# Performance work log

Hardware: AMD Instinct MI355X
Metric: run time of the kernel (lower is better)

The kernel has to match this reference:

```python
import jax, jax.numpy as jnp
import numpy as np

H = 1024          # hidden_size
I = 2048          # intermediate_size
E = 8             # num_experts
K = 2             # num_experts_per_token
B, S = 4, 4096


def setup_inputs() -> dict:
    key = jax.random.key(0)
    ks = jax.random.split(key, 5)
    scale = 0.02
    return {
        "hidden_states": jax.random.normal(ks[0], (B, S, H), dtype=jnp.float32),
        "gate_w": jax.random.normal(ks[1], (H, E), dtype=jnp.float32) * scale,      # router gate (Linear, no bias), stored [in,out]
        "gate_proj_w": jax.random.normal(ks[2], (E, H, I), dtype=jnp.float32) * scale,
        "up_proj_w": jax.random.normal(ks[3], (E, H, I), dtype=jnp.float32) * scale,
        "down_proj_w": jax.random.normal(ks[4], (E, I, H), dtype=jnp.float32) * scale,
    }


def reference(hidden_states, gate_w, gate_proj_w, up_proj_w, down_proj_w):
    b, s, h = hidden_states.shape
    x = hidden_states.reshape(-1, h)                      # (T, H), T = b*s
    T = x.shape[0]

    # --- Router: softmax over experts, top-k, renormalize ---
    logits = x @ gate_w                                    # (T, E)
    probs = jax.nn.softmax(logits, axis=-1)
    topk_w, topk_idx = jax.lax.top_k(probs, K)             # (T, K)
    topk_w = topk_w / jnp.sum(topk_w, axis=-1, keepdims=True)

    # Per-token combine weight for each expert (0 if not routed).
    # topk indices are distinct, so scatter-add == scatter-set here.
    combine = jnp.zeros((T, E), dtype=x.dtype).at[
        jnp.arange(T)[:, None], topk_idx
    ].add(topk_w)                                          # (T, E)

    # --- Experts: SwiGLU FFN, weighted combine ---
    out = jnp.zeros_like(x)
    for e in range(E):  # small fixed expert count
        g = jax.nn.silu(x @ gate_proj_w[e])                # (T, I)
        u = x @ up_proj_w[e]                               # (T, I)
        y = (g * u) @ down_proj_w[e]                       # (T, H)
        out = out + y * combine[:, e:e + 1]
    return out.reshape(b, s, h)
```

## Files before the change

kernel.cpp:

```cpp
#include <hip/hip_runtime.h>
#include <hip/hip_bf16.h>

#define T_TOK 16384
#define H_DIM 1024
#define I_DIM 2048
#define E_NUM 8

typedef short short8 __attribute__((ext_vector_type(8)));
typedef float f32x4 __attribute__((ext_vector_type(4)));

__device__ __forceinline__ unsigned short f2bf(float f) {
  union { float f; unsigned u; } v; v.f = f;
  unsigned r = (v.u + 0x7FFFu + ((v.u >> 16) & 1u)) >> 16;
  return (unsigned short)r;
}
__device__ __forceinline__ float bf2f(unsigned short u) {
  union { unsigned u; float f; } v; v.u = ((unsigned)u) << 16;
  return v.f;
}

__device__ __forceinline__ void gload16(const void* g, void* l) {
  __builtin_amdgcn_global_load_lds(
      (const __attribute__((address_space(1))) unsigned int*)g,
      (__attribute__((address_space(3))) unsigned int*)l, 16, 0, 0);
}

#define VMCNT4() asm volatile("s_waitcnt vmcnt(4)" ::: "memory")
#define VMCNT0() asm volatile("s_waitcnt vmcnt(0)" ::: "memory")
#define BAR() __builtin_amdgcn_s_barrier()
#define SCHEDFENCE() __builtin_amdgcn_sched_barrier(0)
#define PRIO1() __builtin_amdgcn_s_setprio(1)
#define PRIO0() __builtin_amdgcn_s_setprio(0)

__global__ __launch_bounds__(256) void convert_router_kernel(
    const float* __restrict__ x, const float* __restrict__ gw,
    unsigned short* __restrict__ xb,
    int* __restrict__ tke, float* __restrict__ pwv) {
  const int tid = threadIdx.x;
  const int lane = tid & 63;
  const int wv = tid >> 6;
  const int t = blockIdx.x * 4 + wv;
  const float* xr = x + (size_t)t * H_DIM;
  unsigned short* xbr = xb + (size_t)t * H_DIM;

  float acc[8] = {0.f, 0.f, 0.f, 0.f, 0.f, 0.f, 0.f, 0.f};
#pragma unroll
  for (int i = 0; i < 16; ++i) {
    const int h = i * 64 + lane;
    float xv = xr[h];
    xbr[h] = f2bf(xv);
    const float4 g0 = *(const float4*)(gw + (size_t)h * 8);
    const float4 g1 = *(const float4*)(gw + (size_t)h * 8 + 4);
    acc[0] += xv * g0.x; acc[1] += xv * g0.y;
    acc[2] += xv * g0.z; acc[3] += xv * g0.w;
    acc[4] += xv * g1.x; acc[5] += xv * g1.y;
    acc[6] += xv * g1.z; acc[7] += xv * g1.w;
  }
#pragma unroll
  for (int e = 0; e < 8; ++e) {
#pragma unroll
    for (int off = 32; off; off >>= 1) acc[e] += __shfl_xor(acc[e], off);
  }
  int e1 = 0; float l1 = acc[0];
#pragma unroll
  for (int e = 1; e < 8; ++e) if (acc[e] > l1) { l1 = acc[e]; e1 = e; }
  int first_non = (e1 == 0) ? 1 : 0;
  int e2 = first_non; float l2 = acc[first_non];
#pragma unroll
  for (int e = 0; e < 8; ++e) {
    if (e == e1 || e == first_non) continue;
    if (acc[e] > l2) { l2 = acc[e]; e2 = e; }
  }
  float r = expf(l2 - l1);
  float w1 = 1.f / (1.f + r);
  float w2 = r / (1.f + r);
  if (lane == 0) {
    pwv[2 * t] = w1;
    pwv[2 * t + 1] = w2;
    tke[t] = e1 | (e2 << 4);
  }
}

__global__ __launch_bounds__(256) void build_lists_kernel(
    const int* __restrict__ tke, int* __restrict__ list, int* __restrict__ cnt) {
  const int t = blockIdx.x * 256 + threadIdx.x;
  const int lane = threadIdx.x & 63;
  const int pk = tke[t];
  const int ee[2] = {pk & 15, (pk >> 4) & 15};
#pragma unroll
  for (int phase = 0; phase < 2; ++phase) {
    const int e = ee[phase];
    const int pid = 2 * t + phase;
#pragma unroll
    for (int ex = 0; ex < E_NUM; ++ex) {
      unsigned long long mask = __ballot(e == ex);
      if (e == ex) {
        unsigned long long below = mask & ((1ull << lane) - 1ull);
        int rank = __popcll(below);
        int leader = __ffsll((unsigned long long)mask) - 1;
        int base = 0;
        if (lane == leader) base = atomicAdd(&cnt[ex], __popcll(mask));
        base = __shfl(base, leader);
        list[ex * T_TOK + base + rank] = pid;
      }
    }
  }
}

__global__ __launch_bounds__(256) void transpose_convert(
    const float* __restrict__ src, unsigned short* __restrict__ dst, int K, int N) {
  __shared__ float t[128][65];
  const int e = blockIdx.x, kt = blockIdx.y, nt = blockIdx.z;
  const float* s = src + (size_t)e * K * N + (size_t)(kt * 128) * N + nt * 64;
  unsigned short* d = dst + (size_t)e * N * K + (size_t)(nt * 64) * K + kt * 128;
  const int tid = threadIdx.x;
  const int lr = tid & 15, row = tid >> 4;
#pragma unroll
  for (int p = 0; p < 8; ++p) {
    int k = row + p * 16;
    float4 v = *(const float4*)(s + (size_t)k * N + lr * 4);
    t[k][lr * 4 + 0] = v.x;
    t[k][lr * 4 + 1] = v.y;
    t[k][lr * 4 + 2] = v.z;
    t[k][lr * 4 + 3] = v.w;
  }
  __syncthreads();
  const int kc = tid & 15, nr = tid >> 4;
#pragma unroll
  for (int p = 0; p < 4; ++p) {
    int n = nr + p * 16;
    short8 o;
#pragma unroll
    for (int j = 0; j < 8; ++j) o[j] = (short)f2bf(t[kc * 8 + j][n]);
    *(short8*)&d[(size_t)n * K + kc * 8] = o;
  }
}

__global__ __launch_bounds__(256, 3) void gemm_gateup(
    const unsigned short* __restrict__ xb, const unsigned short* __restrict__ wgt,
    const unsigned short* __restrict__ wut, const int* __restrict__ list,
    const int* __restrict__ cnt, const float* __restrict__ pwv,
    unsigned short* __restrict__ hbuf) {
  __shared__ unsigned short As[2][128 * 32];
  __shared__ unsigned short Bg[2][64 * 32];
  __shared__ unsigned short Bu[2][64 * 32];
  __shared__ int rows_s[128];
  __shared__ float pws[128];

  const int tid = threadIdx.x;
  const int e = blockIdx.y >> 7;
  const int mt = blockIdx.y & 127;
  const int ce = cnt[e];
  if (mt * 128 >= ce) return;
  const int n0 = blockIdx.x * 64;

  if (tid < 128) {
    int idx = mt * 128 + tid;
    int pid = list[e * T_TOK + (idx < ce ? idx : 0)];
    rows_s[tid] = pid;
    pws[tid] = pwv[pid];
  }
  __syncthreads();

  const int s0 = tid, s1 = 256 + tid;
  const int q0 = (((s0 & 3) ^ ((s0 >> 3) & 3)) * 8);
  const int q1 = (((s1 & 3) ^ ((s1 >> 3) & 3)) * 8);
  const int tok0 = rows_s[s0 >> 2] >> 1, tok1 = rows_s[s1 >> 2] >> 1;

  const unsigned short* wg_base = wgt + ((size_t)e * I_DIM + n0) * H_DIM;
  const unsigned short* wu_base = wut + ((size_t)e * I_DIM + n0) * H_DIM;
  const unsigned short* a_src0 = xb + (size_t)tok0 * H_DIM + q0;
  const unsigned short* a_src1 = xb + (size_t)tok1 * H_DIM + q1;
  const unsigned short* g_src0 = wg_base + (size_t)(s0 >> 2) * H_DIM + q0;
  const unsigned short* u_src0 = wu_base + (size_t)(s0 >> 2) * H_DIM + q0;

#define STAGE_GU(b, k0)                         \
  do {                                          \
    gload16(a_src0 + (k0), &As[b][s0 * 8]);     \
    gload16(a_src1 + (k0), &As[b][s1 * 8]);     \
    gload16(g_src0 + (k0), &Bg[b][s0 * 8]);     \
    gload16(u_src0 + (k0), &Bu[b][s0 * 8]);     \
  } while (0)

  f32x4 zero = {0.f, 0.f, 0.f, 0.f};
  f32x4 accg[4][2], accu[4][2];
#pragma unroll
  for (int m = 0; m < 4; ++m)
#pragma unroll
    for (int n = 0; n < 2; ++n) { accg[m][n] = zero; accu[m][n] = zero; }

  const int lane = tid & 63;
  const int wv = tid >> 6;
  const int wr = (wv >> 1) * 64;
  const int wc = (wv & 1) * 32;
  const int lr = lane & 15;
  const int lks = (((lane >> 4) ^ ((lr >> 1) & 3)) * 8);

  STAGE_GU(0, 0);

  for (int kt = 0; kt < H_DIM / 32; ++kt) {
    const int cur = kt & 1;
    if (kt < H_DIM / 32 - 1) {
      STAGE_GU(cur ^ 1, (kt + 1) * 32);
      VMCNT4();
    } else {
      VMCNT0();
    }
    BAR();
    SCHEDFENCE();
    const unsigned short* Ab = As[cur];
    const unsigned short* Bgb = Bg[cur];
    const unsigned short* Bub = Bu[cur];
    short8 a[4], bg[2], bu[2];
#pragma unroll
    for (int m = 0; m < 4; ++m)
      a[m] = *(const short8*)&Ab[(wr + m * 16 + lr) * 32 + lks];
#pragma unroll
    for (int n = 0; n < 2; ++n) {
      bg[n] = *(const short8*)&Bgb[(wc + n * 16 + lr) * 32 + lks];
      bu[n] = *(const short8*)&Bub[(wc + n * 16 + lr) * 32 + lks];
    }
    PRIO1();
#pragma unroll
    for (int m = 0; m < 4; ++m)
#pragma unroll
      for (int n = 0; n < 2; ++n) {
        accg[m][n] = __builtin_amdgcn_mfma_f32_16x16x32_bf16(a[m], bg[n], accg[m][n], 0, 0, 0);
        accu[m][n] = __builtin_amdgcn_mfma_f32_16x16x32_bf16(a[m], bu[n], accu[m][n], 0, 0, 0);
      }
    PRIO0();
    BAR();
  }
#undef STAGE_GU

  const int rr = (lane >> 4) * 4;
#pragma unroll
  for (int m = 0; m < 4; ++m) {
#pragma unroll
    for (int j = 0; j < 4; ++j) {
      int tr = wr + m * 16 + rr + j;
      if (mt * 128 + tr < ce) {
        int pid = rows_s[tr];
        float wgt_r = pws[tr];
        size_t rowb = (size_t)pid * I_DIM + n0 + wc;
#pragma unroll
        for (int n = 0; n < 2; ++n) {
          float g = accg[m][n][j];
          float u = accu[m][n][j];
          float hv = wgt_r * (g / (1.f + __expf(-g))) * u;
          hbuf[rowb + n * 16 + lr] = f2bf(hv);
        }
      }
    }
  }
}

__global__ __launch_bounds__(256, 3) void gemm_down(
    const unsigned short* __restrict__ hbuf, const unsigned short* __restrict__ wdt,
    const int* __restrict__ list, const int* __restrict__ cnt,
    unsigned short* __restrict__ pbuf) {
  __shared__ unsigned short As[3][128 * 32];
  __shared__ unsigned short Bs[3][128 * 32];
  __shared__ int rows_s[128];

  const int tid = threadIdx.x;
  const int e = blockIdx.y >> 7;
  const int mt = blockIdx.y & 127;
  const int ce = cnt[e];
  if (mt * 128 >= ce) return;
  const int n0 = blockIdx.x * 128;

  if (tid < 128) {
    int idx = mt * 128 + tid;
    rows_s[tid] = list[e * T_TOK + (idx < ce ? idx : 0)];
  }
  __syncthreads();

  const int s0 = tid, s1 = 256 + tid;
  const int r0s = s0 >> 2, r1s = s1 >> 2;
  const int q0 = (((s0 & 3) ^ ((s0 >> 3) & 3)) * 8);
  const int q1 = (((s1 & 3) ^ ((s1 >> 3) & 3)) * 8);
  const int pid0 = rows_s[r0s], pid1 = rows_s[r1s];

  const unsigned short* wd_base = wdt + ((size_t)e * H_DIM + n0) * I_DIM;
  const unsigned short* a_src0 = hbuf + (size_t)pid0 * I_DIM + q0;
  const unsigned short* a_src1 = hbuf + (size_t)pid1 * I_DIM + q1;
  const unsigned short* b_src0 = wd_base + (size_t)r0s * I_DIM + q0;
  const unsigned short* b_src1 = wd_base + (size_t)r1s * I_DIM + q1;

#define STAGE_DN(b, k0)                         \
  do {                                          \
    gload16(a_src0 + (k0), &As[b][s0 * 8]);     \
    gload16(a_src1 + (k0), &As[b][s1 * 8]);     \
    gload16(b_src0 + (k0), &Bs[b][s0 * 8]);     \
    gload16(b_src1 + (k0), &Bs[b][s1 * 8]);     \
  } while (0)

  f32x4 zero = {0.f, 0.f, 0.f, 0.f};
  f32x4 acc[4][4];
#pragma unroll
  for (int m = 0; m < 4; ++m)
#pragma unroll
    for (int n = 0; n < 4; ++n) acc[m][n] = zero;

  const int lane = tid & 63;
  const int wv = tid >> 6;
  const int wr = (wv >> 1) * 64;
  const int wc = (wv & 1) * 64;
  const int lr = lane & 15;
  const int lks = (((lane >> 4) ^ ((lr >> 1) & 3)) * 8);

  STAGE_DN(0, 0);
  STAGE_DN(1, 32);

  int rb = 0;
  for (int kt = 0; kt < I_DIM / 32; ++kt) {
    if (kt < I_DIM / 32 - 1) VMCNT4(); else VMCNT0();
    BAR();
    SCHEDFENCE();
    if (kt + 2 < I_DIM / 32) {
      int sb = rb + 2; if (sb >= 3) sb -= 3;
      STAGE_DN(sb, (kt + 2) * 32);
    }
    const unsigned short* Ab = As[rb];
    const unsigned short* Bb = Bs[rb];
    short8 a[4], b[4];
#pragma unroll
    for (int m = 0; m < 4; ++m)
      a[m] = *(const short8*)&Ab[(wr + m * 16 + lr) * 32 + lks];
#pragma unroll
    for (int n = 0; n < 4; ++n)
      b[n] = *(const short8*)&Bb[(wc + n * 16 + lr) * 32 + lks];
    PRIO1();
#pragma unroll
    for (int m = 0; m < 4; ++m)
#pragma unroll
      for (int n = 0; n < 4; ++n)
        acc[m][n] = __builtin_amdgcn_mfma_f32_16x16x32_bf16(a[m], b[n], acc[m][n], 0, 0, 0);
    PRIO0();
    rb = (rb + 1 == 3) ? 0 : rb + 1;
  }
#undef STAGE_DN

  const int rr = (lane >> 4) * 4;
#pragma unroll
  for (int m = 0; m < 4; ++m) {
#pragma unroll
    for (int j = 0; j < 4; ++j) {
      int tr = wr + m * 16 + rr + j;
      if (mt * 128 + tr < ce) {
        int pid = rows_s[tr];
        unsigned short* orow = pbuf + (size_t)pid * H_DIM + n0 + wc;
#pragma unroll
        for (int n = 0; n < 4; ++n)
          orow[n * 16 + lr] = f2bf(acc[m][n][j]);
      }
    }
  }
}

__global__ __launch_bounds__(256) void combine_kernel(float* __restrict__ out) {
  const int tid = threadIdx.x, lane = tid & 63, wv = tid >> 6;
  const int t = blockIdx.x * 4 + wv;
  const unsigned short* p = (const unsigned short*)out;
  const unsigned short* r0 = p + (size_t)(2 * t) * H_DIM + lane * 16;
  const unsigned short* r1 = p + (size_t)(2 * t + 1) * H_DIM + lane * 16;
  short8 a0 = *(const short8*)r0;
  short8 a1 = *(const short8*)(r0 + 8);
  short8 b0 = *(const short8*)r1;
  short8 b1 = *(const short8*)(r1 + 8);
  float res[16];
#pragma unroll
  for (int j = 0; j < 8; ++j) {
    res[j] = bf2f((unsigned short)a0[j]) + bf2f((unsigned short)b0[j]);
    res[8 + j] = bf2f((unsigned short)a1[j]) + bf2f((unsigned short)b1[j]);
  }
  float* orow = out + (size_t)t * H_DIM + lane * 16;
#pragma unroll
  for (int j = 0; j < 4; ++j) {
    float4 w = {res[4 * j], res[4 * j + 1], res[4 * j + 2], res[4 * j + 3]};
    ((float4*)orow)[j] = w;
  }
}

extern "C" void kernel_launch(void* const* d_in, const int* in_sizes, int n_in,
                              void* d_out, int out_size, void* d_ws, size_t ws_size,
                              hipStream_t stream) {
  const float* x = (const float*)d_in[0];
  const float* gw = (const float*)d_in[1];
  const float* wgf = (const float*)d_in[2];
  const float* wuf = (const float*)d_in[3];
  const float* wdf = (const float*)d_in[4];

  const size_t off_xb   = 0;
  const size_t off_wdt  = 33554432;
  const size_t off_h    = 67108864;
  const size_t off_list = 201326592;
  const size_t off_pw   = 201850880;
  const size_t off_cnt  = 201981952;
  const size_t ws_needed = off_cnt + 64;
  if (ws_size < ws_needed) return;

  char* ws = (char*)d_ws;
  unsigned short* xb   = (unsigned short*)(ws + off_xb);
  unsigned short* wdt  = (unsigned short*)(ws + off_wdt);
  unsigned short* hbuf = (unsigned short*)(ws + off_h);
  int*   list = (int*)(ws + off_list);
  float* pwv  = (float*)(ws + off_pw);
  int*   cnt  = (int*)(ws + off_cnt);
  int*   tke  = (int*)(ws + off_h);

  unsigned short* wgt = (unsigned short*)d_out;
  unsigned short* wut = (unsigned short*)d_out + (size_t)E_NUM * H_DIM * I_DIM;
  unsigned short* pbuf = (unsigned short*)d_out;

  hipMemsetAsync(cnt, 0, E_NUM * sizeof(int), stream);

  convert_router_kernel<<<T_TOK / 4, 256, 0, stream>>>(x, gw, xb, tke, pwv);
  build_lists_kernel<<<T_TOK / 256, 256, 0, stream>>>(tke, list, cnt);
  transpose_convert<<<dim3(E_NUM, H_DIM / 128, I_DIM / 64), 256, 0, stream>>>(
      wgf, wgt, H_DIM, I_DIM);
  transpose_convert<<<dim3(E_NUM, H_DIM / 128, I_DIM / 64), 256, 0, stream>>>(
      wuf, wut, H_DIM, I_DIM);
  transpose_convert<<<dim3(E_NUM, I_DIM / 128, H_DIM / 64), 256, 0, stream>>>(
      wdf, wdt, I_DIM, H_DIM);

  gemm_gateup<<<dim3(I_DIM / 64, E_NUM * 128), 256, 0, stream>>>(
      xb, wgt, wut, list, cnt, pwv, hbuf);

  gemm_down<<<dim3(H_DIM / 128, E_NUM * 128), 256, 0, stream>>>(
      hbuf, wdt, list, cnt, pbuf);

  combine_kernel<<<T_TOK / 4, 256, 0, stream>>>((float*)d_out);
}
```

Baseline: 707.3 us.

## Load gate/up weight fragments directly into registers, bypassing LDS

The gate/up GEMM no longer stages the weight tiles through shared memory. Each wave loads its B fragments straight from global memory into registers, double-buffered across an unrolled pair of K steps, while the activation tile still goes through LDS via global_load_lds. This removes LDS traffic and LDS footprint for the weights, which could allow higher occupancy. In exchange, weight tiles shared by the waves with the same column offset are now fetched redundantly from global/L2, and the wait-count bookkeeping becomes more fragile.

```diff
diff --git a/kernel.cpp b/kernel.cpp
--- a/kernel.cpp
+++ b/kernel.cpp
@@ -25,6 +25,7 @@
       (__attribute__((address_space(3))) unsigned int*)l, 16, 0, 0);
 }
 
+#define VMCNT6() asm volatile("s_waitcnt vmcnt(6)" ::: "memory")
 #define VMCNT4() asm volatile("s_waitcnt vmcnt(4)" ::: "memory")
 #define VMCNT0() asm volatile("s_waitcnt vmcnt(0)" ::: "memory")
 #define BAR() __builtin_amdgcn_s_barrier()
@@ -142,8 +143,6 @@
     const int* __restrict__ cnt, const float* __restrict__ pwv,
     unsigned short* __restrict__ hbuf) {
   __shared__ unsigned short As[2][128 * 32];
-  __shared__ unsigned short Bg[2][64 * 32];
-  __shared__ unsigned short Bu[2][64 * 32];
   __shared__ int rows_s[128];
   __shared__ float pws[128];
 
@@ -166,74 +165,94 @@
   const int q0 = (((s0 & 3) ^ ((s0 >> 3) & 3)) * 8);
   const int q1 = (((s1 & 3) ^ ((s1 >> 3) & 3)) * 8);
   const int tok0 = rows_s[s0 >> 2] >> 1, tok1 = rows_s[s1 >> 2] >> 1;
-
-  const unsigned short* wg_base = wgt + ((size_t)e * I_DIM + n0) * H_DIM;
-  const unsigned short* wu_base = wut + ((size_t)e * I_DIM + n0) * H_DIM;
   const unsigned short* a_src0 = xb + (size_t)tok0 * H_DIM + q0;
   const unsigned short* a_src1 = xb + (size_t)tok1 * H_DIM + q1;
-  const unsigned short* g_src0 = wg_base + (size_t)(s0 >> 2) * H_DIM + q0;
-  const unsigned short* u_src0 = wu_base + (size_t)(s0 >> 2) * H_DIM + q0;
-
-#define STAGE_GU(b, k0)                         \
+
+#define STAGE_A(b, k0)                          \
   do {                                          \
     gload16(a_src0 + (k0), &As[b][s0 * 8]);     \
     gload16(a_src1 + (k0), &As[b][s1 * 8]);     \
-    gload16(g_src0 + (k0), &Bg[b][s0 * 8]);     \
-    gload16(u_src0 + (k0), &Bu[b][s0 * 8]);     \
   } while (0)
-
-  f32x4 zero = {0.f, 0.f, 0.f, 0.f};
-  f32x4 accg[4][2], accu[4][2];
-#pragma unroll
-  for (int m = 0; m < 4; ++m)
-#pragma unroll
-    for (int n = 0; n < 2; ++n) { accg[m][n] = zero; accu[m][n] = zero; }
 
   const int lane = tid & 63;
   const int wv = tid >> 6;
   const int wr = (wv >> 1) * 64;
   const int wc = (wv & 1) * 32;
   const int lr = lane & 15;
-  const int lks = (((lane >> 4) ^ ((lr >> 1) & 3)) * 8);
-
-  STAGE_GU(0, 0);
-
-  for (int kt = 0; kt < H_DIM / 32; ++kt) {
-    const int cur = kt & 1;
-    if (kt < H_DIM / 32 - 1) {
-      STAGE_GU(cur ^ 1, (kt + 1) * 32);
-      VMCNT4();
-    } else {
-      VMCNT0();
-    }
-    BAR();
-    SCHEDFENCE();
-    const unsigned short* Ab = As[cur];
-    const unsigned short* Bgb = Bg[cur];
-    const unsigned short* Bub = Bu[cur];
-    short8 a[4], bg[2], bu[2];
-#pragma unroll
-    for (int m = 0; m < 4; ++m)
-      a[m] = *(const short8*)&Ab[(wr + m * 16 + lr) * 32 + lks];
-#pragma unroll
-    for (int n = 0; n < 2; ++n) {
-      bg[n] = *(const short8*)&Bgb[(wc + n * 16 + lr) * 32 + lks];
-      bu[n] = *(const short8*)&Bub[(wc + n * 16 + lr) * 32 + lks];
-    }
-    PRIO1();
-#pragma unroll
-    for (int m = 0; m < 4; ++m)
-#pragma unroll
-      for (int n = 0; n < 2; ++n) {
-        accg[m][n] = __builtin_amdgcn_mfma_f32_16x16x32_bf16(a[m], bg[n], accg[m][n], 0, 0, 0);
-        accu[m][n] = __builtin_amdgcn_mfma_f32_16x16x32_bf16(a[m], bu[n], accu[m][n], 0, 0, 0);
+  const int lg = lane >> 4;
+  const int lks = ((lg ^ ((lr >> 1) & 3)) * 8);
+
+  const unsigned short* bg0p = wgt + ((size_t)e * I_DIM + n0 + wc + lr) * H_DIM + lg * 8;
+  const unsigned short* bg1p = bg0p + (size_t)16 * H_DIM;
+  const unsigned short* bu0p = wut + ((size_t)e * I_DIM + n0 + wc + lr) * H_DIM + lg * 8;
+  const unsigned short* bu1p = bu0p + (size_t)16 * H_DIM;
+
+  f32x4 zero = {0.f, 0.f, 0.f, 0.f};
+  f32x4 accg[4][2], accu[4][2];
+#pragma unroll
+  for (int m = 0; m < 4; ++m)
+#pragma unroll
+    for (int n = 0; n < 2; ++n) { accg[m][n] = zero; accu[m][n] = zero; }
+
+  STAGE_A(0, 0);
+  short8 bgA0 = *(const short8*)(bg0p);
+  short8 bgA1 = *(const short8*)(bg1p);
+  short8 buA0 = *(const short8*)(bu0p);
+  short8 buA1 = *(const short8*)(bu1p);
+  short8 bgB0, bgB1, buB0, buB1;
+
+#define GU_MFMA(BG0, BG1, BU0, BU1, AB)                                        \
+  do {                                                                         \
+    short8 a_[4];                                                              \
+    _Pragma("unroll") for (int m = 0; m < 4; ++m)                              \
+        a_[m] = *(const short8*)&(AB)[(wr + m * 16 + lr) * 32 + lks];          \
+    PRIO1();                                                                   \
+    _Pragma("unroll") for (int m = 0; m < 4; ++m) {                            \
+      accg[m][0] = __builtin_amdgcn_mfma_f32_16x16x32_bf16(a_[m], BG0, accg[m][0], 0, 0, 0); \
+      accg[m][1] = __builtin_amdgcn_mfma_f32_16x16x32_bf16(a_[m], BG1, accg[m][1], 0, 0, 0); \
+      accu[m][0] = __builtin_amdgcn_mfma_f32_16x16x32_bf16(a_[m], BU0, accu[m][0], 0, 0, 0); \
+      accu[m][1] = __builtin_amdgcn_mfma_f32_16x16x32_bf16(a_[m], BU1, accu[m][1], 0, 0, 0); \
+    }                                                                          \
+    PRIO0();                                                                   \
+  } while (0)
+
+  for (int kt2 = 0; kt2 < 16; ++kt2) {
+    const int kt = kt2 * 2;
+    {
+      const int k1 = (kt + 1) * 32;
+      STAGE_A(1, k1);
+      bgB0 = *(const short8*)(bg0p + k1);
+      bgB1 = *(const short8*)(bg1p + k1);
+      buB0 = *(const short8*)(bu0p + k1);
+      buB1 = *(const short8*)(bu1p + k1);
+      VMCNT6();
+      BAR();
+      SCHEDFENCE();
+      GU_MFMA(bgA0, bgA1, buA0, buA1, As[0]);
+      BAR();
+    }
+    {
+      if (kt2 < 15) {
+        const int k2 = (kt + 2) * 32;
+        STAGE_A(0, k2);
+        bgA0 = *(const short8*)(bg0p + k2);
+        bgA1 = *(const short8*)(bg1p + k2);
+        buA0 = *(const short8*)(bu0p + k2);
+        buA1 = *(const short8*)(bu1p + k2);
+        VMCNT6();
+      } else {
+        VMCNT0();
       }
-    PRIO0();
-    BAR();
-  }
-#undef STAGE_GU
-
-  const int rr = (lane >> 4) * 4;
+      BAR();
+      SCHEDFENCE();
+      GU_MFMA(bgB0, bgB1, buB0, buB1, As[1]);
+      BAR();
+    }
+  }
+#undef GU_MFMA
+#undef STAGE_A
+
+  const int rr = lg * 4;
 #pragma unroll
   for (int m = 0; m < 4; ++m) {
 #pragma unroll
```

Result: slower. 941.9 us (+33.2%).
